# Kernel tuning notes

Hardware: AMD Instinct MI355X
Metric: run time of the kernel (lower is better)

The kernel has to match this reference:

```python
import jax, jax.numpy as jnp
import numpy as np
from jax import lax

MD = 4  # correlation max displacement -> (2*MD+1)**2 = 81 channels
BACKWARP_COEF = 1.25  # level 4 entry in the coefficient table


def leaky(x):
    return jnp.where(x >= 0, x, 0.1 * x)


def conv3x3(x, w, b):
    # x: [B,Cin,H,W], w: [Cout,Cin,3,3]
    y = lax.conv_general_dilated(x, w, (1, 1), [(1, 1), (1, 1)],
                                 dimension_numbers=('NCHW', 'OIHW', 'NCHW'))
    return y + b[None, :, None, None]


def deconv4x4_s2(x, w, b):
    # torch ConvTranspose2d(k=4, s=2, p=1); w: [Cin,Cout,4,4]
    y = lax.conv_general_dilated(x, w[:, :, ::-1, ::-1], (1, 1), [(2, 2), (2, 2)],
                                 lhs_dilation=(2, 2),
                                 dimension_numbers=('NCHW', 'IOHW', 'NCHW'))
    return y + b[None, :, None, None]


def grid_sample_zeros(img, grid):
    # bilinear, padding_mode='zeros', align_corners=False
    B, C, H, W = img.shape
    x = (grid[..., 0] + 1.0) * 0.5 * W - 0.5  # [B,H,W]
    y = (grid[..., 1] + 1.0) * 0.5 * H - 0.5
    x0 = jnp.floor(x); y0 = jnp.floor(y)
    wx1 = x - x0; wx0 = 1.0 - wx1
    wy1 = y - y0; wy0 = 1.0 - wy1

    def gather(ix, iy):
        valid = (ix >= 0) & (ix < W) & (iy >= 0) & (iy < H)
        ixc = jnp.clip(ix, 0, W - 1).astype(jnp.int32)
        iyc = jnp.clip(iy, 0, H - 1).astype(jnp.int32)
        v = jax.vmap(lambda im, yy, xx: im[:, yy, xx])(img, iyc, ixc)  # [B,C,H,W]
        return jnp.where(valid[:, None], v, 0.0)

    out = (gather(x0, y0) * (wx0 * wy0)[:, None]
           + gather(x0 + 1, y0) * (wx1 * wy0)[:, None]
           + gather(x0, y0 + 1) * (wx0 * wy1)[:, None]
           + gather(x0 + 1, y0 + 1) * (wx1 * wy1)[:, None])
    return out


def backwarp(feat, flow):
    B, C, H, W = feat.shape
    gx = jnp.linspace(-1.0 + 1.0 / W, 1.0 - 1.0 / W, W, dtype=feat.dtype)
    gy = jnp.linspace(-1.0 + 1.0 / H, 1.0 - 1.0 / H, H, dtype=feat.dtype)
    fx = flow[:, 0] / ((W - 1.0) / 2.0)
    fy = flow[:, 1] / ((H - 1.0) / 2.0)
    grid = jnp.stack([gx[None, None, :] + fx, gy[None, :, None] + fy], axis=-1)  # [B,H,W,2]
    feat1 = jnp.concatenate([feat, jnp.ones((B, 1, H, W), feat.dtype)], axis=1)
    out = grid_sample_zeros(feat1, grid)
    mask = jnp.where(out[:, -1:] > 0.999, 1.0, 0.0).astype(feat.dtype)
    return out[:, :-1] * mask


def correlation(f1, f2):
    # PWC-Net cost volume: mean over channels of shifted products, 81 shifts
    B, C, H, W = f1.shape
    f2p = jnp.pad(f2, ((0, 0), (0, 0), (MD, MD), (MD, MD)))
    outs = []
    for dy in range(2 * MD + 1):
        for dx in range(2 * MD + 1):
            outs.append(jnp.mean(f1 * f2p[:, :, dy:dy + H, dx:dx + W], axis=1))
    return jnp.stack(outs, axis=1)  # [B,81,H,W]


def setup_inputs() -> dict:
    key = jax.random.key(0)
    ks = jax.random.split(key, 24)
    B, C, H, W = 16, 48, 64, 128
    cc = 81 + 48 + 2 + 2  # 133
    prev_feat_c = 81 + 48 + 48 + 24 + 16  # 217
    p = lambda k, s: jax.random.normal(k, s, dtype=jnp.float32) * 0.05
    return {
        'feat_1': jax.random.normal(ks[0], (B, C, H, W), dtype=jnp.float32),
        'feat_2': jax.random.normal(ks[1], (B, C, H, W), dtype=jnp.float32),
        'prev_flow': jax.random.normal(ks[2], (B, 2, H // 2, W // 2), dtype=jnp.float32),
        'prev_feat': jax.random.normal(ks[3], (B, prev_feat_c, H // 2, W // 2), dtype=jnp.float32),
        'w1': p(ks[4], (48, cc, 3, 3)), 'b1': p(ks[5], (48,)),
        'w2': p(ks[6], (48, cc + 48, 3, 3)), 'b2': p(ks[7], (48,)),
        'w3': p(ks[8], (24, cc + 96, 3, 3)), 'b3': p(ks[9], (24,)),
        'w4': p(ks[10], (16, cc + 120, 3, 3)), 'b4': p(ks[11], (16,)),
        'w5': p(ks[12], (2, cc + 136, 3, 3)), 'b5': p(ks[13], (2,)),
        'w_upflow': p(ks[14], (2, 2, 4, 4)), 'b_upflow': p(ks[15], (2,)),
        'w_upfeat': p(ks[16], (prev_feat_c, 2, 4, 4)), 'b_upfeat': p(ks[17], (2,)),
    }


def reference(feat_1, feat_2, prev_flow, prev_feat,
              w1, b1, w2, b2, w3, b3, w4, b4, w5, b5,
              w_upflow, b_upflow, w_upfeat, b_upfeat):
    upped_flow = deconv4x4_s2(prev_flow, w_upflow, b_upflow)   # [B,2,H,W]
    upped_feat = deconv4x4_s2(prev_feat, w_upfeat, b_upfeat)   # [B,2,H,W]
    warped_feat_2 = backwarp(feat_2, upped_flow * BACKWARP_COEF)
    corr_volume = leaky(correlation(feat_1, warped_feat_2))    # [B,81,H,W]
    feat_out = jnp.concatenate([corr_volume, feat_1, upped_flow, upped_feat], axis=1)
    feat_out = jnp.concatenate([leaky(conv3x3(feat_out, w1, b1)), feat_out], axis=1)
    feat_out = jnp.concatenate([leaky(conv3x3(feat_out, w2, b2)), feat_out], axis=1)
    feat_out = jnp.concatenate([leaky(conv3x3(feat_out, w3, b3)), feat_out], axis=1)
    feat_out = jnp.concatenate([leaky(conv3x3(feat_out, w4, b4)), feat_out], axis=1)
    flow = leaky(conv3x3(feat_out, w5, b5))
    return flow, feat_out
```

## Files before the change

kernel.cpp:

```cpp
#include <hip/hip_runtime.h>


#define DEVFN __device__ __forceinline__

constexpr int B = 16, H = 64, W = 128, HW = H * W;
constexpr int CF = 48;
constexpr int PFC = 217;
constexpr int H2 = 32, W2 = 64, HW2 = H2 * W2;
constexpr int FC = 269;
constexpr int FCP = 272;
constexpr int FLOW_ELEMS = B * 2 * HW;

constexpr int OFF_CORR = 136, OFF_F1 = 217, OFF_UF = 265, OFF_UPFEAT = 267;
constexpr int FB_F1 = 136, FB_CORR = 184;

constexpr size_t WS_ZEROS = 0;
constexpr size_t WS_FEATB = 256;
constexpr size_t FEATB_BYTES = (size_t)B * HW * FCP * 2;
constexpr size_t WS_WARPEDH = WS_FEATB + FEATB_BYTES;
constexpr size_t WARPEDH_BYTES = (size_t)3 * B * HW * 16 * 2;
constexpr size_t WS_PART = WS_WARPEDH + WARPEDH_BYTES;
constexpr size_t PART_BYTES = (size_t)7 * B * 2 * HW * 4;
constexpr size_t WS_WB = WS_PART + PART_BYTES;

typedef short bf16x8 __attribute__((ext_vector_type(8)));
typedef float f32x4 __attribute__((ext_vector_type(4)));
typedef _Float16 h16x2 __attribute__((ext_vector_type(2)));
typedef _Float16 h16x8 __attribute__((ext_vector_type(8)));

DEVFN float leaky(float x) { return x >= 0.f ? x : 0.1f * x; }

DEVFN unsigned short f2b(float f) {
  unsigned int u = __float_as_uint(f);
  u += 0x7FFFu + ((u >> 16) & 1u);
  return (unsigned short)(u >> 16);
}

DEVFN void gload16(const void* g, void* l) {
  __builtin_amdgcn_global_load_lds(
      (const __attribute__((address_space(1))) void*)g,
      (__attribute__((address_space(3))) void*)l, 16, 0, 0);
}

DEVFN int featb2ref(int p) {
  if (p >= FB_F1 && p < FB_CORR) return OFF_F1 + (p - FB_F1);
  if (p >= FB_CORR && p < 265) return OFF_CORR + (p - FB_CORR);
  return p;
}

__global__ void k_deconv_flow(const float* __restrict__ pflow,
                              const float* __restrict__ wuf,
                              const float* __restrict__ buf_,
                              float* __restrict__ feat,
                              unsigned short* __restrict__ featb) {
  int t = blockIdx.x * blockDim.x + threadIdx.x;
  if (t >= B * 2 * HW) return;
  int x = t % W, y = (t / W) % H, co = (t / HW) % 2, b = t / (2 * HW);
  float acc = buf_[co];
  int ky0 = ((y & 1) == 0) ? 1 : 0;
  int kx0 = ((x & 1) == 0) ? 1 : 0;
#pragma unroll
  for (int kyi = 0; kyi < 2; ++kyi) {
    int ky = ky0 + 2 * kyi;
    int iy = (y + 1 - ky) >> 1;
    if (iy < 0 || iy >= H2) continue;
#pragma unroll
    for (int kxi = 0; kxi < 2; ++kxi) {
      int kx = kx0 + 2 * kxi;
      int ix = (x + 1 - kx) >> 1;
      if (ix < 0 || ix >= W2) continue;
#pragma unroll
      for (int ci = 0; ci < 2; ++ci)
        acc += pflow[(b * 2 + ci) * HW2 + iy * W2 + ix] *
               wuf[((ci * 2 + co) * 4 + ky) * 4 + kx];
    }
  }
  int pix = (b * H + y) * W + x;
  feat[(b * FC + OFF_UF + co) * HW + y * W + x] = acc;
  featb[pix * FCP + OFF_UF + co] = f2b(acc);
  if (co == 0) {
    featb[pix * FCP + 269] = 0;
    featb[pix * FCP + 270] = 0;
    featb[pix * FCP + 271] = 0;
  }
}

__global__ __launch_bounds__(256) void k_dcf_part(
    const float* __restrict__ pfeat, const float* __restrict__ wup,
    float* __restrict__ partial) {
  __shared__ float wl[1024];
  __shared__ float red[2048];
  int blk = blockIdx.x;
  int chunk = blk % 7, t2 = blk / 7;
  int y2 = t2 % H2, b = t2 / H2;
  int tid = threadIdx.x;
  int ch0 = chunk * 32;
  for (int i = tid; i < 1024; i += 256) {
    int ci = ch0 + (i >> 5);
    wl[i] = (ci < PFC) ? wup[ci * 32 + (i & 31)] : 0.f;
  }
  __syncthreads();
  int x2 = tid & 63, cg = tid >> 6;
  float acc[8];
#pragma unroll
  for (int v = 0; v < 8; ++v) acc[v] = 0.f;
#pragma unroll 1
  for (int k = 0; k < 8; ++k) {
    int cil = cg * 8 + k;
    int ci = ch0 + cil;
    bool cv = ci < PFC;
    const float* src = pfeat + ((size_t)b * PFC + ci) * HW2;
    float iv[3][3];
#pragma unroll
    for (int dy = -1; dy <= 1; ++dy)
#pragma unroll
      for (int dx = -1; dx <= 1; ++dx) {
        int iy = y2 + dy, ix = x2 + dx;
        float v = 0.f;
        if (cv && iy >= 0 && iy < H2 && ix >= 0 && ix < W2) v = src[iy * W2 + ix];
        iv[dy + 1][dx + 1] = v;
      }
    const float* wc = &wl[cil * 32];
#pragma unroll
    for (int co = 0; co < 2; ++co)
#pragma unroll
      for (int ry = 0; ry < 2; ++ry)
#pragma unroll
        for (int rx = 0; rx < 2; ++rx) {
          float s = acc[co * 4 + ry * 2 + rx];
#pragma unroll
          for (int dy = ry - 1; dy <= ry; ++dy) {
            int ky = 1 + ry - 2 * dy;
#pragma unroll
            for (int dx = rx - 1; dx <= rx; ++dx) {
              int kx = 1 + rx - 2 * dx;
              s += iv[dy + 1][dx + 1] * wc[co * 16 + ky * 4 + kx];
            }
          }
          acc[co * 4 + ry * 2 + rx] = s;
        }
  }
#pragma unroll
  for (int v = 0; v < 8; ++v) red[(cg * 64 + x2) * 8 + v] = acc[v];
  __syncthreads();
  for (int idx = tid; idx < 512; idx += 256) {
    int x2b = idx & 63, vi = idx >> 6;
    float s = red[(0 + x2b) * 8 + vi] + red[(64 + x2b) * 8 + vi] +
              red[(128 + x2b) * 8 + vi] + red[(192 + x2b) * 8 + vi];
    int co = vi >> 2, ry = (vi >> 1) & 1, rx = vi & 1;
    partial[(size_t)chunk * (B * 2 * HW) + (size_t)(b * 2 + co) * HW +
            (2 * y2 + ry) * W + (2 * x2b + rx)] = s;
  }
}

__global__ void k_fin_upfeat(const float* __restrict__ partial,
                             const float* __restrict__ bup,
                             float* __restrict__ feat,
                             unsigned short* __restrict__ featb) {
  int t = blockIdx.x * 256 + threadIdx.x;
  if (t >= B * 2 * HW) return;
  float s = 0.f;
#pragma unroll
  for (int c = 0; c < 7; ++c) s += partial[(size_t)c * (B * 2 * HW) + t];
  int rem = t % HW;
  int co = (t / HW) & 1;
  int b = t / (2 * HW);
  s += bup[co];
  feat[((size_t)b * FC + OFF_UPFEAT + co) * HW + rem] = s;
  featb[((size_t)(b * H) * W + rem) * FCP + OFF_UPFEAT + co] = f2b(s);
}

__global__ __launch_bounds__(256) void k_backwarp(const float* __restrict__ feat2,
                                                  const float* __restrict__ feat,
                                                  unsigned short* __restrict__ warpedh) {
  int t = blockIdx.x * 256 + threadIdx.x;
  if (t >= B * HW) return;
  int x = t % W, y = (t / W) % H, b = t / HW;
  const float SX = 1.25f * (float)W / (float)(W - 1);
  const float SY = 1.25f * (float)H / (float)(H - 1);
  float fx = feat[(b * FC + OFF_UF + 0) * HW + y * W + x];
  float fy = feat[(b * FC + OFF_UF + 1) * HW + y * W + x];
  float px = (float)x + fx * SX;
  float py = (float)y + fy * SY;
  float x0f = floorf(px), y0f = floorf(py);
  int ix0 = (int)x0f, iy0 = (int)y0f;
  float wx1 = px - x0f, wx0 = 1.f - wx1;
  float wy1 = py - y0f, wy0 = 1.f - wy1;
  bool vx0 = (ix0 >= 0) & (ix0 < W), vx1 = (ix0 + 1 >= 0) & (ix0 + 1 < W);
  bool vy0 = (iy0 >= 0) & (iy0 < H), vy1 = (iy0 + 1 >= 0) & (iy0 + 1 < H);
  float w00 = (vx0 && vy0) ? wx0 * wy0 : 0.f;
  float w01 = (vx1 && vy0) ? wx1 * wy0 : 0.f;
  float w10 = (vx0 && vy1) ? wx0 * wy1 : 0.f;
  float w11 = (vx1 && vy1) ? wx1 * wy1 : 0.f;
  float wsum = w00 + w01 + w10 + w11;
  float m = wsum > 0.999f ? 1.f : 0.f;
  w00 *= m; w01 *= m; w10 *= m; w11 *= m;
  int cx0 = min(max(ix0, 0), W - 1), cx1 = min(max(ix0 + 1, 0), W - 1);
  int cy0 = min(max(iy0, 0), H - 1), cy1 = min(max(iy0 + 1, 0), H - 1);
  const float* s = feat2 + b * CF * HW;
  int o00 = cy0 * W + cx0, o01 = cy0 * W + cx1, o10 = cy1 * W + cx0, o11 = cy1 * W + cx1;
#pragma unroll 1
  for (int chunk = 0; chunk < 3; ++chunk) {
    h16x8 out0, out1;
#pragma unroll
    for (int k = 0; k < 16; ++k) {
      const float* sc = s + (chunk * 16 + k) * HW;
      float v = w00 * sc[o00] + w01 * sc[o01] + w10 * sc[o10] + w11 * sc[o11];
      if (k < 8) out0[k & 7] = (_Float16)v;
      else       out1[k & 7] = (_Float16)v;
    }
    h16x8* dst = (h16x8*)(warpedh + ((size_t)chunk * B * HW + t) * 16);
    dst[0] = out0;
    dst[1] = out1;
  }
}

__global__ __launch_bounds__(256) void k_corr(const float* __restrict__ f1,
                                              const unsigned short* __restrict__ warpedh,
                                              const unsigned short* __restrict__ zeros,
                                              float* __restrict__ feat,
                                              unsigned short* __restrict__ featb) {
  __shared__ __align__(16) unsigned short lds[5 * 136 * 16];
  const int swz = ((blockIdx.x & 7) << 7) | (blockIdx.x >> 3);
  const int y = swz & 63, b = swz >> 6;
  const int tid = threadIdx.x;
  const int px = tid >> 1, h = tid & 1;
  const int lane = tid & 63, wv = tid >> 6;
  const int pix = (b * H + y) * W + px;
  const h16x8* hp = (const h16x8*)lds;
  char* ldsc = (char*)lds;
  const float inv = 1.f / 48.f;

#pragma unroll 1
  for (int half = 0; half < 2; ++half) {
    const int R = half ? 4 : 5;
    const int dybase = half ? 5 : 0;
    const int ND = R * 9;
    float acc[45];
#pragma unroll
    for (int d = 0; d < 45; ++d) acc[d] = 0.f;
#pragma unroll 1
    for (int chunk = 0; chunk < 3; ++chunk) {
      __syncthreads();
      const int NQ = R * 136 * 2;
      for (int q0 = 0; q0 < NQ; q0 += 256) {
        int q = q0 + tid;
        if (q < NQ) {
          int pr = q >> 1, u = q & 1;
          int r = pr / 136, p = pr - r * 136;
          int sw = (p >> 2) & 1;
          int yy = y + dybase + r - 4, xx = p - 4;
          const unsigned short* src = zeros;
          if (yy >= 0 && yy < H && xx >= 0 && xx < W)
            src = warpedh + (((size_t)chunk * B * H + b * H + yy) * W + xx) * 16 +
                  (u ^ sw) * 8;
          gload16(src, ldsc + (size_t)q0 * 16 + wv * 1024 + lane * 16);
        }
      }
      float av[8];
      const int c0 = chunk * 16 + h * 8;
#pragma unroll
      for (int j = 0; j < 8; ++j)
        av[j] = f1[((size_t)b * CF + c0 + j) * HW + y * W + px];
      h16x2 fh[4];
#pragma unroll
      for (int j = 0; j < 4; ++j) {
        fh[j][0] = (_Float16)av[2 * j];
        fh[j][1] = (_Float16)av[2 * j + 1];
      }
      asm volatile("s_waitcnt vmcnt(0)" ::: "memory");
      __syncthreads();
      if (half == 0) {
#pragma unroll
        for (int j = 0; j < 8; ++j)
          feat[((size_t)b * FC + OFF_F1 + c0 + j) * HW + y * W + px] = av[j];
        uint4 qv;
        qv.x = (unsigned)f2b(av[0]) | ((unsigned)f2b(av[1]) << 16);
        qv.y = (unsigned)f2b(av[2]) | ((unsigned)f2b(av[3]) << 16);
        qv.z = (unsigned)f2b(av[4]) | ((unsigned)f2b(av[5]) << 16);
        qv.w = (unsigned)f2b(av[6]) | ((unsigned)f2b(av[7]) << 16);
        *(uint4*)(featb + (size_t)pix * FCP + FB_F1 + c0) = qv;
      }
#pragma unroll
      for (int dy = 0; dy < 5; ++dy) {
        if (dy < R) {
#pragma unroll
          for (int dx = 0; dx < 9; ++dx) {
            int p = px + dx;
            int sw = (p >> 2) & 1;
            h16x8 v = hp[((dy * 136 + p) << 1) | (h ^ sw)];
            float a = acc[dy * 9 + dx];
            a = __builtin_amdgcn_fdot2((h16x2){v[0], v[1]}, fh[0], a, false);
            a = __builtin_amdgcn_fdot2((h16x2){v[2], v[3]}, fh[1], a, false);
            a = __builtin_amdgcn_fdot2((h16x2){v[4], v[5]}, fh[2], a, false);
            a = __builtin_amdgcn_fdot2((h16x2){v[6], v[7]}, fh[3], a, false);
            acc[dy * 9 + dx] = a;
          }
        }
      }
    }
#pragma unroll
    for (int d = 0; d < 45; ++d) {
      if (d < ND) {
        float s = acc[d] + __shfl_xor(acc[d], 1);
        acc[d] = leaky(s * inv);
      }
    }
    if (h == 0) {
#pragma unroll
      for (int d = 0; d < 45; ++d)
        if (d < ND)
          feat[((size_t)b * FC + OFF_CORR + dybase * 9 + d) * HW + y * W + px] = acc[d];
    } else {
      unsigned short* fb = featb + (size_t)pix * FCP + FB_CORR + dybase * 9;
      if (half == 0) {
#pragma unroll
        for (int g = 0; g < 5; ++g) {
          uint4 qv;
          qv.x = (unsigned)f2b(acc[8 * g + 0]) | ((unsigned)f2b(acc[8 * g + 1]) << 16);
          qv.y = (unsigned)f2b(acc[8 * g + 2]) | ((unsigned)f2b(acc[8 * g + 3]) << 16);
          qv.z = (unsigned)f2b(acc[8 * g + 4]) | ((unsigned)f2b(acc[8 * g + 5]) << 16);
          qv.w = (unsigned)f2b(acc[8 * g + 6]) | ((unsigned)f2b(acc[8 * g + 7]) << 16);
          *(uint4*)(fb + 8 * g) = qv;
        }
#pragma unroll
        for (int d = 40; d < 45; ++d) fb[d] = f2b(acc[d]);
      } else {
        fb[0] = f2b(acc[0]);
        fb[1] = f2b(acc[1]);
        fb[2] = f2b(acc[2]);
#pragma unroll
        for (int g = 0; g < 4; ++g) {
          uint4 qv;
          qv.x = (unsigned)f2b(acc[3 + 8 * g + 0]) | ((unsigned)f2b(acc[3 + 8 * g + 1]) << 16);
          qv.y = (unsigned)f2b(acc[3 + 8 * g + 2]) | ((unsigned)f2b(acc[3 + 8 * g + 3]) << 16);
          qv.z = (unsigned)f2b(acc[3 + 8 * g + 4]) | ((unsigned)f2b(acc[3 + 8 * g + 5]) << 16);
          qv.w = (unsigned)f2b(acc[3 + 8 * g + 6]) | ((unsigned)f2b(acc[3 + 8 * g + 7]) << 16);
          *(uint4*)(fb + 3 + 8 * g) = qv;
        }
        fb[35] = f2b(acc[35]);
      }
    }
  }
}

template <int CIN, int NCHUNK, int COUT, int COUTP, int IN_OFF>
__global__ void k_repack(const float* __restrict__ w, unsigned short* __restrict__ wb) {
  int e = blockIdx.x * 256 + threadIdx.x;
  constexpr int TOT = NCHUNK * 9 * COUTP * 32;
  if (e >= TOT) return;
  int j = e & 7, qpos = (e >> 3) & 3;
  int row = e >> 5;
  int co = row % COUTP;
  int tapch = row / COUTP;
  int tap = tapch % 9, ch = tapch / 9;
  int k = ch * 32 + ((qpos ^ ((co >> 1) & 3)) << 3) + j;
  float v = 0.f;
  if (co < COUT && k < CIN) {
    int ci = featb2ref(IN_OFF + k) - IN_OFF;
    v = w[(co * CIN + ci) * 9 + tap];
  }
  wb[e] = f2b(v);
}

template <int CIN, int NCHUNK, int COUT, int COUTP, int IN_OFF, int OUT_OFF, bool TO_FLOW>
__global__ __launch_bounds__(256) void k_conv_mfma(
    const unsigned short* __restrict__ featb, const unsigned short* __restrict__ wb,
    const float* __restrict__ bias, const unsigned short* __restrict__ zeros,
    float* __restrict__ fout, unsigned short* __restrict__ bout) {
  constexpr int NF = COUTP / 16;
  constexpr int ROWPX = 144;
  constexpr int IN_ELE = 3 * ROWPX * 32;
  constexpr int W_SLAB = 9 * COUTP * 32;
  constexpr int NIN = 27;
  constexpr int NWI = (W_SLAB * 2) / 1024;
  constexpr int NINST = NIN + NWI;
  constexpr int MYI = (NINST + 3) / 4;
  constexpr int CLIM = 264 - IN_OFF;

  __shared__ unsigned short lds[IN_ELE + W_SLAB];

  const int swz = ((blockIdx.x & 7) << 7) | (blockIdx.x >> 3);
  const int y = swz % H, b = swz / H;
  const int lane = threadIdx.x & 63, wv = threadIdx.x >> 6;
  const int arow = lane & 15, aslc = lane >> 4;

  const unsigned short* gp[MYI];
  int c8a[MYI];
  int lofs[MYI];
  bool iw[MYI];
#pragma unroll
  for (int t = 0; t < MYI; ++t) {
    int i = wv + t * 4;
    gp[t] = zeros; c8a[t] = 1 << 20; lofs[t] = 0; iw[t] = false;
    if (i < NIN) {
      int r = i / 9, seg = i - r * 9;
      int slot = seg * 16 + (lane >> 2);
      int sub8 = ((lane & 3) ^ ((slot >> 1) & 3)) << 3;
      int yy = y + r - 1, xx = slot - 1;
      lofs[t] = (r * ROWPX + seg * 16) * 64;
      if (yy >= 0 && yy < H && xx >= 0 && xx < W) {
        gp[t] = featb + ((b * H + yy) * W + xx) * FCP + IN_OFF + sub8;
        c8a[t] = sub8;
      }
    } else if (i < NINST) {
      int wi = i - NIN;
      iw[t] = true;
      gp[t] = wb + wi * 512 + lane * 8;
      lofs[t] = IN_ELE * 2 + wi * 1024;
    }
  }

  int a_off[2][3];
#pragma unroll
  for (int mi = 0; mi < 2; ++mi)
#pragma unroll
    for (int kx = 0; kx < 3; ++kx) {
      int slot = (wv * 2 + mi) * 16 + arow + kx;
      a_off[mi][kx] = slot * 32 + ((aslc ^ ((slot >> 1) & 3)) << 3);
    }
  int b_off[NF];
#pragma unroll
  for (int nf = 0; nf < NF; ++nf) {
    int co = nf * 16 + arow;
    b_off[nf] = IN_ELE + co * 32 + ((aslc ^ ((co >> 1) & 3)) << 3);
  }

  f32x4 acc[2][NF];
#pragma unroll
  for (int mi = 0; mi < 2; ++mi)
#pragma unroll
    for (int nf = 0; nf < NF; ++nf) acc[mi][nf] = (f32x4){0.f, 0.f, 0.f, 0.f};

  char* ldsc = (char*)lds;

  for (int ch = 0; ch < NCHUNK; ++ch) {
    const int ci0 = ch * 32;
    __syncthreads();
#pragma unroll
    for (int t = 0; t < MYI; ++t) {
      int i = wv + t * 4;
      if (i < NINST) {
        const unsigned short* g;
        if (iw[t]) g = gp[t] + (size_t)ch * W_SLAB;
        else       g = (c8a[t] + ci0 <= CLIM) ? gp[t] + ci0 : zeros;
        gload16(g, ldsc + lofs[t]);
      }
    }
    asm volatile("s_waitcnt vmcnt(0)" ::: "memory");
    __syncthreads();
#pragma unroll
    for (int ky = 0; ky < 3; ++ky) {
#pragma unroll
      for (int kx = 0; kx < 3; ++kx) {
        bf16x8 afr[2];
#pragma unroll
        for (int mi = 0; mi < 2; ++mi)
          afr[mi] = *(const bf16x8*)(lds + a_off[mi][kx] + ky * (ROWPX * 32));
#pragma unroll
        for (int nf = 0; nf < NF; ++nf) {
          bf16x8 bfr = *(const bf16x8*)(lds + b_off[nf] + (ky * 3 + kx) * (COUTP * 32));
#pragma unroll
          for (int mi = 0; mi < 2; ++mi)
            acc[mi][nf] = __builtin_amdgcn_mfma_f32_16x16x32_bf16(
                afr[mi], bfr, acc[mi][nf], 0, 0, 0);
        }
      }
    }
  }

  const int dcol = lane & 15;
#pragma unroll
  for (int nf = 0; nf < NF; ++nf) {
    int co = nf * 16 + dcol;
    if (co < COUT) {
      float bv = bias[co];
#pragma unroll
      for (int mi = 0; mi < 2; ++mi) {
#pragma unroll
        for (int r = 0; r < 4; ++r) {
          int pixel = (wv * 2 + mi) * 16 + (lane >> 4) * 4 + r;
          float v = leaky(acc[mi][nf][r] + bv);
          if constexpr (TO_FLOW) {
            fout[(b * 2 + co) * HW + y * W + pixel] = v;
          } else {
            fout[(b * FC + OUT_OFF + co) * HW + y * W + pixel] = v;
            bout[((b * H + y) * W + pixel) * FCP + OUT_OFF + co] = f2b(v);
          }
        }
      }
    }
  }
}

extern "C" void kernel_launch(void* const* d_in, const int* in_sizes, int n_in,
                              void* d_out, int out_size, void* d_ws, size_t ws_size,
                              hipStream_t stream) {
  (void)in_sizes; (void)n_in; (void)out_size; (void)ws_size;
  const float* feat_1 = (const float*)d_in[0];
  const float* feat_2 = (const float*)d_in[1];
  const float* prev_flow = (const float*)d_in[2];
  const float* prev_feat = (const float*)d_in[3];
  const float* w1 = (const float*)d_in[4];
  const float* b1 = (const float*)d_in[5];
  const float* w2 = (const float*)d_in[6];
  const float* b2 = (const float*)d_in[7];
  const float* w3 = (const float*)d_in[8];
  const float* b3 = (const float*)d_in[9];
  const float* w4 = (const float*)d_in[10];
  const float* b4 = (const float*)d_in[11];
  const float* w5 = (const float*)d_in[12];
  const float* b5 = (const float*)d_in[13];
  const float* w_upflow = (const float*)d_in[14];
  const float* b_upflow = (const float*)d_in[15];
  const float* w_upfeat = (const float*)d_in[16];
  const float* b_upfeat = (const float*)d_in[17];

  float* out = (float*)d_out;
  float* feat = out + FLOW_ELEMS;

  char* ws = (char*)d_ws;
  unsigned short* zeros = (unsigned short*)(ws + WS_ZEROS);
  unsigned short* featb = (unsigned short*)(ws + WS_FEATB);
  unsigned short* warpedh = (unsigned short*)(ws + WS_WARPEDH);
  float* partial = (float*)(ws + WS_PART);
  unsigned short* wb1 = (unsigned short*)(ws + WS_WB);
  unsigned short* wb2 = wb1 + 5 * 9 * 48 * 32;
  unsigned short* wb3 = wb2 + 6 * 9 * 48 * 32;
  unsigned short* wb4 = wb3 + 8 * 9 * 32 * 32;
  unsigned short* wb5 = wb4 + 8 * 9 * 16 * 32;

  hipMemsetAsync(zeros, 0, 64, stream);

  k_repack<133, 5, 48, 48, 136><<<270, 256, 0, stream>>>(w1, wb1);
  k_repack<181, 6, 48, 48, 88><<<324, 256, 0, stream>>>(w2, wb2);
  k_repack<229, 8, 24, 32, 40><<<288, 256, 0, stream>>>(w3, wb3);
  k_repack<253, 8, 16, 16, 16><<<144, 256, 0, stream>>>(w4, wb4);
  k_repack<269, 9, 2, 16, 0><<<162, 256, 0, stream>>>(w5, wb5);

  k_deconv_flow<<<(B * 2 * HW) / 256, 256, 0, stream>>>(prev_flow, w_upflow, b_upflow, feat, featb);
  k_dcf_part<<<B * H2 * 7, 256, 0, stream>>>(prev_feat, w_upfeat, partial);
  k_fin_upfeat<<<(B * 2 * HW) / 256, 256, 0, stream>>>(partial, b_upfeat, feat, featb);
  k_backwarp<<<(B * HW) / 256, 256, 0, stream>>>(feat_2, feat, warpedh);
  k_corr<<<B * H, 256, 0, stream>>>(feat_1, warpedh, zeros, feat, featb);

  k_conv_mfma<133, 5, 48, 48, 136, 88, false><<<B * H, 256, 0, stream>>>(featb, wb1, b1, zeros, feat, featb);
  k_conv_mfma<181, 6, 48, 48, 88, 40, false><<<B * H, 256, 0, stream>>>(featb, wb2, b2, zeros, feat, featb);
  k_conv_mfma<229, 8, 24, 32, 40, 16, false><<<B * H, 256, 0, stream>>>(featb, wb3, b3, zeros, feat, featb);
  k_conv_mfma<253, 8, 16, 16, 16, 0, false><<<B * H, 256, 0, stream>>>(featb, wb4, b4, zeros, feat, featb);
  k_conv_mfma<269, 9, 2, 16, 0, 0, true><<<B * H, 256, 0, stream>>>(featb, wb5, b5, zeros, out, nullptr);
}
```

Before: 296.1 us.

## Merge prologue kernels and compute two output rows per conv block

Combines the five weight-repack launches and the zero memset into one kernel. It merges deconv-flow with the upfeat partial kernel, and the upfeat finalize with backwarp, to cut launch count and idle tails. The MFMA conv kernels now process two image rows per block, loading four input rows into LDS instead of three, so halo reads are reused across rows and the weight slab is shared by twice as many pixels. Each wave holds four M-fragments, which raises register use and halves the grid size. That can lower occupancy.

After: 247.7 us. 16.3% less time.

```diff
diff --git a/kernel.cpp b/kernel.cpp
--- a/kernel.cpp
+++ b/kernel.cpp
@@ -48,52 +48,85 @@
   return p;
 }
 
-__global__ void k_deconv_flow(const float* __restrict__ pflow,
-                              const float* __restrict__ wuf,
-                              const float* __restrict__ buf_,
-                              float* __restrict__ feat,
-                              unsigned short* __restrict__ featb) {
-  int t = blockIdx.x * blockDim.x + threadIdx.x;
-  if (t >= B * 2 * HW) return;
-  int x = t % W, y = (t / W) % H, co = (t / HW) % 2, b = t / (2 * HW);
-  float acc = buf_[co];
-  int ky0 = ((y & 1) == 0) ? 1 : 0;
-  int kx0 = ((x & 1) == 0) ? 1 : 0;
-#pragma unroll
-  for (int kyi = 0; kyi < 2; ++kyi) {
-    int ky = ky0 + 2 * kyi;
-    int iy = (y + 1 - ky) >> 1;
-    if (iy < 0 || iy >= H2) continue;
-#pragma unroll
-    for (int kxi = 0; kxi < 2; ++kxi) {
-      int kx = kx0 + 2 * kxi;
-      int ix = (x + 1 - kx) >> 1;
-      if (ix < 0 || ix >= W2) continue;
-#pragma unroll
-      for (int ci = 0; ci < 2; ++ci)
-        acc += pflow[(b * 2 + ci) * HW2 + iy * W2 + ix] *
-               wuf[((ci * 2 + co) * 4 + ky) * 4 + kx];
-    }
-  }
-  int pix = (b * H + y) * W + x;
-  feat[(b * FC + OFF_UF + co) * HW + y * W + x] = acc;
-  featb[pix * FCP + OFF_UF + co] = f2b(acc);
-  if (co == 0) {
-    featb[pix * FCP + 269] = 0;
-    featb[pix * FCP + 270] = 0;
-    featb[pix * FCP + 271] = 0;
-  }
-}
-
-__global__ __launch_bounds__(256) void k_dcf_part(
+__global__ __launch_bounds__(256) void k_repack_all(
+    const float* __restrict__ w1, const float* __restrict__ w2,
+    const float* __restrict__ w3, const float* __restrict__ w4,
+    const float* __restrict__ w5,
+    unsigned short* __restrict__ wb1, unsigned short* __restrict__ wb2,
+    unsigned short* __restrict__ wb3, unsigned short* __restrict__ wb4,
+    unsigned short* __restrict__ wb5, unsigned short* __restrict__ zeros) {
+  int blk = blockIdx.x;
+  if (blk == 0 && threadIdx.x < 32) zeros[threadIdx.x] = 0;
+  const float* w;
+  unsigned short* wb;
+  int CIN, COUT, COUTP, IN_OFF, rbase;
+  if (blk < 270)       { w = w1; wb = wb1; CIN = 133; COUT = 48; COUTP = 48; IN_OFF = 136; rbase = 0; }
+  else if (blk < 594)  { w = w2; wb = wb2; CIN = 181; COUT = 48; COUTP = 48; IN_OFF = 88;  rbase = 270; }
+  else if (blk < 882)  { w = w3; wb = wb3; CIN = 229; COUT = 24; COUTP = 32; IN_OFF = 40;  rbase = 594; }
+  else if (blk < 1026) { w = w4; wb = wb4; CIN = 253; COUT = 16; COUTP = 16; IN_OFF = 16;  rbase = 882; }
+  else                 { w = w5; wb = wb5; CIN = 269; COUT = 2;  COUTP = 16; IN_OFF = 0;   rbase = 1026; }
+  int e = (blk - rbase) * 256 + threadIdx.x;
+  int nchunk = (CIN + 31) >> 5;
+  int TOT = nchunk * 9 * COUTP * 32;
+  if (e >= TOT) return;
+  int j = e & 7, qpos = (e >> 3) & 3;
+  int row = e >> 5;
+  int co = row % COUTP;
+  int tapch = row / COUTP;
+  int tap = tapch % 9, ch = tapch / 9;
+  int k = ch * 32 + ((qpos ^ ((co >> 1) & 3)) << 3) + j;
+  float v = 0.f;
+  if (co < COUT && k < CIN) {
+    int ci = featb2ref(IN_OFF + k) - IN_OFF;
+    v = w[(co * CIN + ci) * 9 + tap];
+  }
+  wb[e] = f2b(v);
+}
+
+__global__ __launch_bounds__(256) void k_dcf_dflow(
     const float* __restrict__ pfeat, const float* __restrict__ wup,
-    float* __restrict__ partial) {
+    const float* __restrict__ pflow, const float* __restrict__ wuf,
+    const float* __restrict__ buf_, float* __restrict__ partial,
+    float* __restrict__ feat, unsigned short* __restrict__ featb) {
   __shared__ float wl[1024];
   __shared__ float red[2048];
+  int tid = threadIdx.x;
+  if (blockIdx.x >= 3584) {
+    int t = (blockIdx.x - 3584) * 256 + tid;
+    if (t >= B * 2 * HW) return;
+    int x = t % W, y = (t / W) % H, co = (t / HW) % 2, b = t / (2 * HW);
+    float acc = buf_[co];
+    int ky0 = ((y & 1) == 0) ? 1 : 0;
+    int kx0 = ((x & 1) == 0) ? 1 : 0;
+#pragma unroll
+    for (int kyi = 0; kyi < 2; ++kyi) {
+      int ky = ky0 + 2 * kyi;
+      int iy = (y + 1 - ky) >> 1;
+      if (iy < 0 || iy >= H2) continue;
+#pragma unroll
+      for (int kxi = 0; kxi < 2; ++kxi) {
+        int kx = kx0 + 2 * kxi;
+        int ix = (x + 1 - kx) >> 1;
+        if (ix < 0 || ix >= W2) continue;
+#pragma unroll
+        for (int ci = 0; ci < 2; ++ci)
+          acc += pflow[(b * 2 + ci) * HW2 + iy * W2 + ix] *
+                 wuf[((ci * 2 + co) * 4 + ky) * 4 + kx];
+      }
+    }
+    int pix = (b * H + y) * W + x;
+    feat[(b * FC + OFF_UF + co) * HW + y * W + x] = acc;
+    featb[pix * FCP + OFF_UF + co] = f2b(acc);
+    if (co == 0) {
+      featb[pix * FCP + 269] = 0;
+      featb[pix * FCP + 270] = 0;
+      featb[pix * FCP + 271] = 0;
+    }
+    return;
+  }
   int blk = blockIdx.x;
   int chunk = blk % 7, t2 = blk / 7;
   int y2 = t2 % H2, b = t2 / H2;
-  int tid = threadIdx.x;
   int ch0 = chunk * 32;
   for (int i = tid; i < 1024; i += 256) {
     int ci = ch0 + (i >> 5);
@@ -153,27 +186,25 @@
   }
 }
 
-__global__ void k_fin_upfeat(const float* __restrict__ partial,
-                             const float* __restrict__ bup,
-                             float* __restrict__ feat,
-                             unsigned short* __restrict__ featb) {
-  int t = blockIdx.x * 256 + threadIdx.x;
-  if (t >= B * 2 * HW) return;
-  float s = 0.f;
-#pragma unroll
-  for (int c = 0; c < 7; ++c) s += partial[(size_t)c * (B * 2 * HW) + t];
-  int rem = t % HW;
-  int co = (t / HW) & 1;
-  int b = t / (2 * HW);
-  s += bup[co];
-  feat[((size_t)b * FC + OFF_UPFEAT + co) * HW + rem] = s;
-  featb[((size_t)(b * H) * W + rem) * FCP + OFF_UPFEAT + co] = f2b(s);
-}
-
-__global__ __launch_bounds__(256) void k_backwarp(const float* __restrict__ feat2,
-                                                  const float* __restrict__ feat,
-                                                  unsigned short* __restrict__ warpedh) {
-  int t = blockIdx.x * 256 + threadIdx.x;
+__global__ __launch_bounds__(256) void k_fin_backwarp(
+    const float* __restrict__ partial, const float* __restrict__ bup,
+    const float* __restrict__ feat2, float* __restrict__ feat,
+    unsigned short* __restrict__ featb, unsigned short* __restrict__ warpedh) {
+  int tid = threadIdx.x;
+  if (blockIdx.x < 1024) {
+    int t = blockIdx.x * 256 + tid;
+    float s = 0.f;
+#pragma unroll
+    for (int c = 0; c < 7; ++c) s += partial[(size_t)c * (B * 2 * HW) + t];
+    int rem = t % HW;
+    int co = (t / HW) & 1;
+    int b = t / (2 * HW);
+    s += bup[co];
+    feat[((size_t)b * FC + OFF_UPFEAT + co) * HW + rem] = s;
+    featb[((size_t)(b * H) * W + rem) * FCP + OFF_UPFEAT + co] = f2b(s);
+    return;
+  }
+  int t = (blockIdx.x - 1024) * 256 + tid;
   if (t >= B * HW) return;
   int x = t % W, y = (t / W) % H, b = t / HW;
   const float SX = 1.25f * (float)W / (float)(W - 1);
@@ -344,25 +375,6 @@
   }
 }
 
-template <int CIN, int NCHUNK, int COUT, int COUTP, int IN_OFF>
-__global__ void k_repack(const float* __restrict__ w, unsigned short* __restrict__ wb) {
-  int e = blockIdx.x * 256 + threadIdx.x;
-  constexpr int TOT = NCHUNK * 9 * COUTP * 32;
-  if (e >= TOT) return;
-  int j = e & 7, qpos = (e >> 3) & 3;
-  int row = e >> 5;
-  int co = row % COUTP;
-  int tapch = row / COUTP;
-  int tap = tapch % 9, ch = tapch / 9;
-  int k = ch * 32 + ((qpos ^ ((co >> 1) & 3)) << 3) + j;
-  float v = 0.f;
-  if (co < COUT && k < CIN) {
-    int ci = featb2ref(IN_OFF + k) - IN_OFF;
-    v = w[(co * CIN + ci) * 9 + tap];
-  }
-  wb[e] = f2b(v);
-}
-
 template <int CIN, int NCHUNK, int COUT, int COUTP, int IN_OFF, int OUT_OFF, bool TO_FLOW>
 __global__ __launch_bounds__(256) void k_conv_mfma(
     const unsigned short* __restrict__ featb, const unsigned short* __restrict__ wb,
@@ -370,53 +382,43 @@
     float* __restrict__ fout, unsigned short* __restrict__ bout) {
   constexpr int NF = COUTP / 16;
   constexpr int ROWPX = 144;
-  constexpr int IN_ELE = 3 * ROWPX * 32;
+  constexpr int IN_ELE = 4 * ROWPX * 32;
   constexpr int W_SLAB = 9 * COUTP * 32;
-  constexpr int NIN = 27;
   constexpr int NWI = (W_SLAB * 2) / 1024;
-  constexpr int NINST = NIN + NWI;
-  constexpr int MYI = (NINST + 3) / 4;
   constexpr int CLIM = 264 - IN_OFF;
 
   __shared__ unsigned short lds[IN_ELE + W_SLAB];
 
-  const int swz = ((blockIdx.x & 7) << 7) | (blockIdx.x >> 3);
-  const int y = swz % H, b = swz / H;
+  const int swz = ((blockIdx.x & 7) << 6) | (blockIdx.x >> 3);
+  const int y0 = (swz & 31) * 2, b = swz >> 5;
   const int lane = threadIdx.x & 63, wv = threadIdx.x >> 6;
+  const int wr = wv >> 1, wc = wv & 1;
   const int arow = lane & 15, aslc = lane >> 4;
 
-  const unsigned short* gp[MYI];
-  int c8a[MYI];
-  int lofs[MYI];
-  bool iw[MYI];
-#pragma unroll
-  for (int t = 0; t < MYI; ++t) {
+  const unsigned short* gp[9];
+  int c8a[9];
+  int lofs[9];
+#pragma unroll
+  for (int t = 0; t < 9; ++t) {
     int i = wv + t * 4;
-    gp[t] = zeros; c8a[t] = 1 << 20; lofs[t] = 0; iw[t] = false;
-    if (i < NIN) {
-      int r = i / 9, seg = i - r * 9;
-      int slot = seg * 16 + (lane >> 2);
-      int sub8 = ((lane & 3) ^ ((slot >> 1) & 3)) << 3;
-      int yy = y + r - 1, xx = slot - 1;
-      lofs[t] = (r * ROWPX + seg * 16) * 64;
-      if (yy >= 0 && yy < H && xx >= 0 && xx < W) {
-        gp[t] = featb + ((b * H + yy) * W + xx) * FCP + IN_OFF + sub8;
-        c8a[t] = sub8;
-      }
-    } else if (i < NINST) {
-      int wi = i - NIN;
-      iw[t] = true;
-      gp[t] = wb + wi * 512 + lane * 8;
-      lofs[t] = IN_ELE * 2 + wi * 1024;
-    }
-  }
-
-  int a_off[2][3];
-#pragma unroll
-  for (int mi = 0; mi < 2; ++mi)
+    int r = i / 9, seg = i - r * 9;
+    int slot = seg * 16 + (lane >> 2);
+    int sub8 = ((lane & 3) ^ ((slot >> 1) & 3)) << 3;
+    int yy = y0 + r - 1, xx = slot - 1;
+    lofs[t] = (r * ROWPX + seg * 16) * 64;
+    gp[t] = zeros; c8a[t] = 1 << 20;
+    if (yy >= 0 && yy < H && xx >= 0 && xx < W) {
+      gp[t] = featb + ((b * H + yy) * W + xx) * FCP + IN_OFF + sub8;
+      c8a[t] = sub8;
+    }
+  }
+
+  int a_off[4][3];
+#pragma unroll
+  for (int mi = 0; mi < 4; ++mi)
 #pragma unroll
     for (int kx = 0; kx < 3; ++kx) {
-      int slot = (wv * 2 + mi) * 16 + arow + kx;
+      int slot = (wc * 4 + mi) * 16 + arow + kx;
       a_off[mi][kx] = slot * 32 + ((aslc ^ ((slot >> 1) & 3)) << 3);
     }
   int b_off[NF];
@@ -426,9 +428,9 @@
     b_off[nf] = IN_ELE + co * 32 + ((aslc ^ ((co >> 1) & 3)) << 3);
   }
 
-  f32x4 acc[2][NF];
-#pragma unroll
-  for (int mi = 0; mi < 2; ++mi)
+  f32x4 acc[4][NF];
+#pragma unroll
+  for (int mi = 0; mi < 4; ++mi)
 #pragma unroll
     for (int nf = 0; nf < NF; ++nf) acc[mi][nf] = (f32x4){0.f, 0.f, 0.f, 0.f};
 
@@ -438,30 +440,28 @@
     const int ci0 = ch * 32;
     __syncthreads();
 #pragma unroll
-    for (int t = 0; t < MYI; ++t) {
-      int i = wv + t * 4;
-      if (i < NINST) {
-        const unsigned short* g;
-        if (iw[t]) g = gp[t] + (size_t)ch * W_SLAB;
-        else       g = (c8a[t] + ci0 <= CLIM) ? gp[t] + ci0 : zeros;
-        gload16(g, ldsc + lofs[t]);
-      }
-    }
+    for (int t = 0; t < 9; ++t) {
+      const unsigned short* g = (c8a[t] + ci0 <= CLIM) ? gp[t] + ci0 : zeros;
+      gload16(g, ldsc + lofs[t]);
+    }
+    for (int wi = wv; wi < NWI; wi += 4)
+      gload16(wb + (size_t)ch * W_SLAB + wi * 512 + lane * 8,
+              ldsc + IN_ELE * 2 + wi * 1024);
     asm volatile("s_waitcnt vmcnt(0)" ::: "memory");
     __syncthreads();
 #pragma unroll
     for (int ky = 0; ky < 3; ++ky) {
 #pragma unroll
       for (int kx = 0; kx < 3; ++kx) {
-        bf16x8 afr[2];
-#pragma unroll
-        for (int mi = 0; mi < 2; ++mi)
-          afr[mi] = *(const bf16x8*)(lds + a_off[mi][kx] + ky * (ROWPX * 32));
+        bf16x8 afr[4];
+#pragma unroll
+        for (int mi = 0; mi < 4; ++mi)
+          afr[mi] = *(const bf16x8*)(lds + a_off[mi][kx] + (wr + ky) * (ROWPX * 32));
 #pragma unroll
         for (int nf = 0; nf < NF; ++nf) {
           bf16x8 bfr = *(const bf16x8*)(lds + b_off[nf] + (ky * 3 + kx) * (COUTP * 32));
 #pragma unroll
-          for (int mi = 0; mi < 2; ++mi)
+          for (int mi = 0; mi < 4; ++mi)
             acc[mi][nf] = __builtin_amdgcn_mfma_f32_16x16x32_bf16(
                 afr[mi], bfr, acc[mi][nf], 0, 0, 0);
         }
@@ -470,22 +470,23 @@
   }
 
   const int dcol = lane & 15;
+  const int yout = y0 + wr;
 #pragma unroll
   for (int nf = 0; nf < NF; ++nf) {
     int co = nf * 16 + dcol;
     if (co < COUT) {
       float bv = bias[co];
 #pragma unroll
-      for (int mi = 0; mi < 2; ++mi) {
+      for (int mi = 0; mi < 4; ++mi) {
 #pragma unroll
         for (int r = 0; r < 4; ++r) {
-          int pixel = (wv * 2 + mi) * 16 + (lane >> 4) * 4 + r;
+          int pixel = (wc * 4 + mi) * 16 + (lane >> 4) * 4 + r;
           float v = leaky(acc[mi][nf][r] + bv);
           if constexpr (TO_FLOW) {
-            fout[(b * 2 + co) * HW + y * W + pixel] = v;
+            fout[(b * 2 + co) * HW + yout * W + pixel] = v;
           } else {
-            fout[(b * FC + OUT_OFF + co) * HW + y * W + pixel] = v;
-            bout[((b * H + y) * W + pixel) * FCP + OUT_OFF + co] = f2b(v);
+            fout[(b * FC + OUT_OFF + co) * HW + yout * W + pixel] = v;
+            bout[((b * H + yout) * W + pixel) * FCP + OUT_OFF + co] = f2b(v);
           }
         }
       }
@@ -530,23 +531,17 @@
   unsigned short* wb4 = wb3 + 8 * 9 * 32 * 32;
   unsigned short* wb5 = wb4 + 8 * 9 * 16 * 32;
 
-  hipMemsetAsync(zeros, 0, 64, stream);
-
-  k_repack<133, 5, 48, 48, 136><<<270, 256, 0, stream>>>(w1, wb1);
-  k_repack<181, 6, 48, 48, 88><<<324, 256, 0, stream>>>(w2, wb2);
-  k_repack<229, 8, 24, 32, 40><<<288, 256, 0, stream>>>(w3, wb3);
-  k_repack<253, 8, 16, 16, 16><<<144, 256, 0, stream>>>(w4, wb4);
-  k_repack<269, 9, 2, 16, 0><<<162, 256, 0, stream>>>(w5, wb5);
-
-  k_deconv_flow<<<(B * 2 * HW) / 256, 256, 0, stream>>>(prev_flow, w_upflow, b_upflow, feat, featb);
-  k_dcf_part<<<B * H2 * 7, 256, 0, stream>>>(prev_feat, w_upfeat, partial);
-  k_fin_upfeat<<<(B * 2 * HW) / 256, 256, 0, stream>>>(partial, b_upfeat, feat, featb);
-  k_backwarp<<<(B * HW) / 256, 256, 0, stream>>>(feat_2, feat, warpedh);
+  k_repack_all<<<1188, 256, 0, stream>>>(w1, w2, w3, w4, w5,
+                                         wb1, wb2, wb3, wb4, wb5, zeros);
+  k_dcf_dflow<<<3584 + 1024, 256, 0, stream>>>(prev_feat, w_upfeat, prev_flow,
+                                               w_upflow, b_upflow, partial, feat, featb);
+  k_fin_backwarp<<<1024 + 512, 256, 0, stream>>>(partial, b_upfeat, feat_2,
+                                                 feat, featb, warpedh);
   k_corr<<<B * H, 256, 0, stream>>>(feat_1, warpedh, zeros, feat, featb);
 
-  k_conv_mfma<133, 5, 48, 48, 136, 88, false><<<B * H, 256, 0, stream>>>(featb, wb1, b1, zeros, feat, featb);
-  k_conv_mfma<181, 6, 48, 48, 88, 40, false><<<B * H, 256, 0, stream>>>(featb, wb2, b2, zeros, feat, featb);
-  k_conv_mfma<229, 8, 24, 32, 40, 16, false><<<B * H, 256, 0, stream>>>(featb, wb3, b3, zeros, feat, featb);
-  k_conv_mfma<253, 8, 16, 16, 16, 0, false><<<B * H, 256, 0, stream>>>(featb, wb4, b4, zeros, feat, featb);
-  k_conv_mfma<269, 9, 2, 16, 0, 0, true><<<B * H, 256, 0, stream>>>(featb, wb5, b5, zeros, out, nullptr);
-}
+  k_conv_mfma<133, 5, 48, 48, 136, 88, false><<<B * H / 2, 256, 0, stream>>>(featb, wb1, b1, zeros, feat, featb);
+  k_conv_mfma<181, 6, 48, 48, 88, 40, false><<<B * H / 2, 256, 0, stream>>>(featb, wb2, b2, zeros, feat, featb);
+  k_conv_mfma<229, 8, 24, 32, 40, 16, false><<<B * H / 2, 256, 0, stream>>>(featb, wb3, b3, zeros, feat, featb);
+  k_conv_mfma<253, 8, 16, 16, 16, 0, false><<<B * H / 2, 256, 0, stream>>>(featb, wb4, b4, zeros, feat, featb);
+  k_conv_mfma<269, 9, 2, 16, 0, 0, true><<<B * H / 2, 256, 0, stream>>>(featb, wb5, b5, zeros, out, nullptr);
+}
```
